# Kernel optimization log

Hardware: AMD Instinct MI355X
Metric: run time of the kernel (lower is better)

The kernel has to match this reference:

```python
import jax, jax.numpy as jnp
import numpy as np

D = 768          # hidden_size
N_HEADS = 12
HEAD_DIM = D // N_HEADS  # 64
WINDOW = 128 // 2        # local_attention // 2 = 64 tokens each side
ROPE_THETA = 10000.0     # local_rope_theta


def _rope_freqs(T, dtype=jnp.float32):
    # complex rotation factors e^{i * pos * inv_freq}, shape [T, HEAD_DIM//2]
    inv_freq = 1.0 / (ROPE_THETA ** (jnp.arange(0, HEAD_DIM, 2, dtype=dtype) / HEAD_DIM))
    ang = jnp.arange(T, dtype=dtype)[:, None] * inv_freq[None, :]
    return jnp.exp(1j * ang.astype(jnp.complex64))


def _apply_rope(x, freqs):
    # x: [B, T, N, H]; split into (2, H//2) pairs as in the source reshape
    B, T, N, H = x.shape
    pairs = x.reshape(B, T, N, 2, H // 2)
    c = pairs[..., 0, :] + 1j * pairs[..., 1, :]          # [B,T,N,H//2]
    rot = c * freqs[None, :, None, :]                      # broadcast over B, heads
    out = jnp.stack([jnp.real(rot), jnp.imag(rot)], axis=-1)  # [B,T,N,H//2,2]
    return out.reshape(B, T, N, H)  # attention_scaling = 1.0 for default rope


def setup_inputs() -> dict:
    key = jax.random.key(0)
    k1, k2, k3 = jax.random.split(key, 3)
    B, T = 4, 2048
    hidden_states = jax.random.normal(k1, (B, T, D), dtype=jnp.float32)
    attention_mask = jnp.ones((B, T), dtype=jnp.int32)
    Wqkv = jax.random.normal(k2, (3 * D, D), dtype=jnp.float32) * (1.0 / np.sqrt(D))
    Wo = jax.random.normal(k3, (D, D), dtype=jnp.float32) * (1.0 / np.sqrt(D))
    return {"hidden_states": hidden_states, "attention_mask": attention_mask,
            "Wqkv": Wqkv, "Wo": Wo}


def reference(hidden_states, attention_mask, Wqkv, Wo):
    B, T, _ = hidden_states.shape
    # fused QKV projection (no bias in ModernBERT)
    qkv = jnp.einsum('btd,ed->bte', hidden_states, Wqkv)   # [B,T,3D]
    q, k, v = jnp.split(qkv, 3, axis=-1)
    to_heads = lambda x: x.reshape(B, T, N_HEADS, HEAD_DIM)
    q, k, v = to_heads(q), to_heads(k), to_heads(v)
    # rotary embedding (complex multiply)
    freqs = _rope_freqs(T)
    q = _apply_rope(q, freqs)
    k = _apply_rope(k, freqs)
    # sliding-window + padding mask
    pos = jnp.arange(T)
    window = jnp.abs(pos[:, None] - pos[None, :]) <= WINDOW   # [T,T]
    pad = attention_mask.astype(jnp.bool_)                    # [B,T]
    allowed = window[None, None, :, :] & pad[:, None, :, None] & pad[:, None, None, :]
    # eager SDPA
    scale = 1.0 / np.sqrt(HEAD_DIM)
    scores = jnp.einsum('bqnh,bknh->bnqk', q, k) * scale      # [B,N,T,T]
    scores = jnp.where(allowed, scores, jnp.finfo(scores.dtype).min)
    probs = jax.nn.softmax(scores, axis=-1)
    attn = jnp.einsum('bnqk,bknh->bqnh', probs, v)            # [B,T,N,H]
    attn = attn.reshape(B, T, D)
    return jnp.einsum('btd,ed->bte', attn, Wo)                # output proj
```

## Files before the change

kernel.cpp:

```cpp
#include <hip/hip_runtime.h>
#include <hip/hip_bf16.h>
#include <math.h>

#define BATCH 4
#define SEQ   2048
#define DMODEL 768
#define NHEADS 12
#define HDIM  64
#define WIN   64
#define QKV_LD 2304

typedef __attribute__((ext_vector_type(8))) short bf16x8;
typedef __attribute__((ext_vector_type(4))) float f32x4;

typedef __attribute__((address_space(1))) const unsigned int guint;
typedef __attribute__((address_space(3))) unsigned int luint;

__device__ inline void gl_lds16(const __hip_bfloat16* g, __hip_bfloat16* l) {
    __builtin_amdgcn_global_load_lds((guint*)g, (luint*)l, 16, 0, 0);
}

__device__ inline void to_out(float* p, float v) { *p = v; }
__device__ inline void to_out(__hip_bfloat16* p, float v) { *p = __float2bfloat16(v); }

#define N4_HID  (BATCH * SEQ * DMODEL / 4)
#define N4_WQKV (QKV_LD * DMODEL / 4)
#define N4_WO   (DMODEL * DMODEL / 4)
#define N_ROPE  (SEQ * 32)
#define SETUP_TOTAL (N4_HID + N4_WQKV + N4_WO + N_ROPE)

__device__ inline void cast4(const float* in, __hip_bfloat16* out, int i) {
    float4 v = ((const float4*)in)[i];
    union { ushort4 u; __hip_bfloat16 h[4]; } o;
    o.h[0] = __float2bfloat16(v.x); o.h[1] = __float2bfloat16(v.y);
    o.h[2] = __float2bfloat16(v.z); o.h[3] = __float2bfloat16(v.w);
    ((ushort4*)out)[i] = o.u;
}

__global__ __launch_bounds__(256) void setup_kernel(const float* __restrict__ hidden,
                                                    const float* __restrict__ Wqkv,
                                                    const float* __restrict__ Wo,
                                                    __hip_bfloat16* __restrict__ hid_bf,
                                                    __hip_bfloat16* __restrict__ wqkv_bf,
                                                    __hip_bfloat16* __restrict__ wo_bf,
                                                    float2* __restrict__ tab) {
    int id = blockIdx.x * 256 + threadIdx.x;
    if (id < N4_HID) {
        cast4(hidden, hid_bf, id);
    } else if (id < N4_HID + N4_WQKV) {
        cast4(Wqkv, wqkv_bf, id - N4_HID);
    } else if (id < N4_HID + N4_WQKV + N4_WO) {
        cast4(Wo, wo_bf, id - N4_HID - N4_WQKV);
    } else if (id < SETUP_TOTAL) {
        int idx = id - (N4_HID + N4_WQKV + N4_WO);
        int t = idx >> 5, j = idx & 31;
        const float L2T_OVER_32 = 13.287712379549449f / 32.0f;
        float inv = exp2f(-(float)j * L2T_OVER_32);
        float s, c;
        sincosf((float)t * inv, &s, &c);
        tab[idx] = make_float2(c, s);
    }
}

template <typename OutT, bool ROPE>
__global__ __launch_bounds__(512) void gemm_pipe(const __hip_bfloat16* __restrict__ A,
                                                 const __hip_bfloat16* __restrict__ B,
                                                 OutT* __restrict__ C,
                                                 int lda, int ldb, int ldc,
                                                 const float2* __restrict__ rope_tab) {
    __shared__ __align__(16) char smem[131072];
    __hip_bfloat16* As = (__hip_bfloat16*)smem;
    __hip_bfloat16* Bs = (__hip_bfloat16*)(smem + 65536);

    const int tid  = threadIdx.x;
    const int lane = tid & 63;
    const int wave = tid >> 6;
    const int wm   = wave >> 1;
    const int wn   = wave & 1;
    const int fr   = lane & 15;
    const int quad = lane >> 4;

    const int bid = blockIdx.x;
    const int x   = bid & 7;
    const int j   = bid >> 3;
    const int m0  = (x * 8 + (j & 7)) * 128;
    const int n0  = (j >> 3) * 128;

    f32x4 acc[2][4];
#pragma unroll
    for (int i = 0; i < 2; i++)
#pragma unroll
        for (int jj = 0; jj < 4; jj++) acc[i][jj] = (f32x4){0.f, 0.f, 0.f, 0.f};

    auto stage = [&](int t) {
        const int s  = t & 3;
        const int k0 = t * 64;
#pragma unroll
        for (int c = 0; c < 2; ++c) {
            int tc  = c * 512 + tid;
            int row = tc >> 3, ch = tc & 7;
            int gcol = (ch ^ (row & 7)) * 8;
            gl_lds16(A + (size_t)(m0 + row) * lda + k0 + gcol, As + s * 8192 + tc * 8);
            gl_lds16(B + (size_t)(n0 + row) * ldb + k0 + gcol, Bs + s * 8192 + tc * 8);
        }
    };

    stage(0); stage(1); stage(2);

#pragma unroll
    for (int t = 0; t < 12; ++t) {
        if (t < 10)       asm volatile("s_waitcnt vmcnt(8)" ::: "memory");
        else if (t == 10) asm volatile("s_waitcnt vmcnt(4)" ::: "memory");
        else              asm volatile("s_waitcnt vmcnt(0)" ::: "memory");
        __builtin_amdgcn_s_barrier();
        __builtin_amdgcn_sched_barrier(0);

        if (t < 9) stage(t + 3);

        const __hip_bfloat16* as = As + (t & 3) * 8192;
        const __hip_bfloat16* bs = Bs + (t & 3) * 8192;
        bf16x8 af[2][2], bfv[2][4];
#pragma unroll
        for (int ks = 0; ks < 2; ++ks) {
#pragma unroll
            for (int mi = 0; mi < 2; ++mi) {
                int row = wm * 32 + mi * 16 + fr;
                int pos = (ks * 4 + quad) ^ (row & 7);
                af[ks][mi] = *(const bf16x8*)(as + row * 64 + pos * 8);
            }
#pragma unroll
            for (int ni = 0; ni < 4; ++ni) {
                int row = wn * 64 + ni * 16 + fr;
                int pos = (ks * 4 + quad) ^ (row & 7);
                bfv[ks][ni] = *(const bf16x8*)(bs + row * 64 + pos * 8);
            }
        }

        __builtin_amdgcn_s_setprio(1);
#pragma unroll
        for (int ks = 0; ks < 2; ++ks)
#pragma unroll
            for (int mi = 0; mi < 2; ++mi)
#pragma unroll
                for (int ni = 0; ni < 4; ++ni)
                    acc[mi][ni] = __builtin_amdgcn_mfma_f32_16x16x32_bf16(af[ks][mi], bfv[ks][ni], acc[mi][ni], 0, 0, 0);
        __builtin_amdgcn_s_setprio(0);
    }

    const int b0 = n0 + wn * 64;
    if (ROPE && b0 < 2 * DMODEL) {
#pragma unroll
        for (int mi = 0; mi < 2; mi++) {
#pragma unroll
            for (int r = 0; r < 4; r++) {
                int t = (m0 + wm * 32 + mi * 16 + quad * 4 + r) & (SEQ - 1);
#pragma unroll
                for (int ni = 0; ni < 2; ni++) {
                    float2 cs = rope_tab[t * 32 + ni * 16 + fr];
                    float x0 = acc[mi][ni][r], x1 = acc[mi][ni + 2][r];
                    acc[mi][ni][r]     = x0 * cs.x - x1 * cs.y;
                    acc[mi][ni + 2][r] = x0 * cs.y + x1 * cs.x;
                }
            }
        }
    }

#pragma unroll
    for (int mi = 0; mi < 2; mi++)
#pragma unroll
        for (int ni = 0; ni < 4; ni++) {
            f32x4 v = acc[mi][ni];
            int gc = b0 + ni * 16 + fr;
            size_t rbase = (size_t)(m0 + wm * 32 + mi * 16 + quad * 4);
#pragma unroll
            for (int r = 0; r < 4; r++)
                to_out(&C[(rbase + r) * ldc + gc], v[r]);
        }
}

#define PLD  192

__global__ __launch_bounds__(256) void attn_kernel(const __hip_bfloat16* __restrict__ qkv,
                                                   const int* __restrict__ mask,
                                                   __hip_bfloat16* __restrict__ attn) {
    __shared__ __align__(16) char smem[49152];
    __hip_bfloat16* Ks = (__hip_bfloat16*)smem;
    __hip_bfloat16* Pb = (__hip_bfloat16*)smem;
    __hip_bfloat16* Vt = (__hip_bfloat16*)(smem + 24576);

    const int tid  = threadIdx.x;
    const int lane = tid & 63;
    const int wave = tid >> 6;
    const int fr   = lane & 15;
    const int quad = lane >> 4;

    const int bid  = blockIdx.x;
    const int x    = bid & 7;
    const int j    = bid >> 3;
    const int b    = x >> 1;
    const int q0   = ((x & 1) * 16 + (j & 15)) * 64;
    const int head = j >> 4;

    const int klo = max(0, q0 - WIN);
    const int khi = min(SEQ, q0 + 64 + WIN);
    const int nk  = khi - klo;
    const int nt  = nk >> 4;
    const int nkc = nk >> 5;

    const size_t rowbase = (size_t)(b * SEQ) * QKV_LD + head * HDIM;

    for (int task = tid; task < nk * 8; task += 256) {
        int row = task >> 3, g = task & 7;
        uint4 v = *(const uint4*)(qkv + rowbase + (size_t)(klo + row) * QKV_LD + DMODEL + g * 8);
        *(uint4*)(Ks + row * 64 + (g ^ (row & 7)) * 8) = v;
    }
    {
        int h = lane;
        const __hip_bfloat16* vb = qkv + rowbase + 2 * DMODEL + h;
        int ng = nk >> 3;
        for (int g = wave; g < ng; g += 4) {
            unsigned int u0, u1, u2, u3;
            {
                unsigned short a0 = *(const unsigned short*)(vb + (size_t)(klo + g * 8 + 0) * QKV_LD);
                unsigned short a1 = *(const unsigned short*)(vb + (size_t)(klo + g * 8 + 1) * QKV_LD);
                unsigned short a2 = *(const unsigned short*)(vb + (size_t)(klo + g * 8 + 2) * QKV_LD);
                unsigned short a3 = *(const unsigned short*)(vb + (size_t)(klo + g * 8 + 3) * QKV_LD);
                unsigned short a4 = *(const unsigned short*)(vb + (size_t)(klo + g * 8 + 4) * QKV_LD);
                unsigned short a5 = *(const unsigned short*)(vb + (size_t)(klo + g * 8 + 5) * QKV_LD);
                unsigned short a6 = *(const unsigned short*)(vb + (size_t)(klo + g * 8 + 6) * QKV_LD);
                unsigned short a7 = *(const unsigned short*)(vb + (size_t)(klo + g * 8 + 7) * QKV_LD);
                u0 = (unsigned int)a0 | ((unsigned int)a1 << 16);
                u1 = (unsigned int)a2 | ((unsigned int)a3 << 16);
                u2 = (unsigned int)a4 | ((unsigned int)a5 << 16);
                u3 = (unsigned int)a6 | ((unsigned int)a7 << 16);
            }
            int cs = g ^ (h & 7);
            *(uint4*)(Vt + h * PLD + cs * 8) = make_uint4(u0, u1, u2, u3);
        }
    }

    const int qrow0 = q0 + wave * 16;
    bf16x8 aq0 = *(const bf16x8*)(qkv + rowbase + (size_t)(qrow0 + fr) * QKV_LD + quad * 8);
    bf16x8 aq1 = *(const bf16x8*)(qkv + rowbase + (size_t)(qrow0 + fr) * QKV_LD + 32 + quad * 8);

    const int* mb = mask + b * SEQ;
    int mq[4];
#pragma unroll
    for (int r = 0; r < 4; r++) mq[r] = mb[qrow0 + quad * 4 + r];

    __syncthreads();

    f32x4 sc[12];
#pragma unroll
    for (int kt = 0; kt < 12; kt++) sc[kt] = (f32x4){-1e30f, -1e30f, -1e30f, -1e30f};

#pragma unroll
    for (int kt = 0; kt < 12; kt++) {
        if (kt < nt) {
            int krow = kt * 16 + fr;
            int kg = klo + krow;
            int p0 = (quad) ^ (krow & 7);
            int p1 = (4 + quad) ^ (krow & 7);
            bf16x8 bk0 = *(const bf16x8*)(Ks + krow * 64 + p0 * 8);
            bf16x8 bk1 = *(const bf16x8*)(Ks + krow * 64 + p1 * 8);
            f32x4 a = (f32x4){0.f, 0.f, 0.f, 0.f};
            a = __builtin_amdgcn_mfma_f32_16x16x32_bf16(aq0, bk0, a, 0, 0, 0);
            a = __builtin_amdgcn_mfma_f32_16x16x32_bf16(aq1, bk1, a, 0, 0, 0);
            int mk = mb[kg];
            f32x4 s;
#pragma unroll
            for (int r = 0; r < 4; r++) {
                int qg = qrow0 + quad * 4 + r;
                bool ok = (abs(qg - kg) <= WIN) && (mk != 0) && (mq[r] != 0);
                s[r] = ok ? a[r] * 0.125f : -1e30f;
            }
            sc[kt] = s;
        }
    }

    f32x4 mx = sc[0];
#pragma unroll
    for (int kt = 1; kt < 12; kt++)
#pragma unroll
        for (int r = 0; r < 4; r++) mx[r] = fmaxf(mx[r], sc[kt][r]);
#pragma unroll
    for (int off = 8; off >= 1; off >>= 1)
#pragma unroll
        for (int r = 0; r < 4; r++) mx[r] = fmaxf(mx[r], __shfl_xor(mx[r], off));

    f32x4 sum = (f32x4){0.f, 0.f, 0.f, 0.f};
#pragma unroll
    for (int kt = 0; kt < 12; kt++)
#pragma unroll
        for (int r = 0; r < 4; r++) {
            float e = __expf(sc[kt][r] - mx[r]);
            sc[kt][r] = e;
            sum[r] += e;
        }
#pragma unroll
    for (int off = 8; off >= 1; off >>= 1)
#pragma unroll
        for (int r = 0; r < 4; r++) sum[r] += __shfl_xor(sum[r], off);
    f32x4 rs;
#pragma unroll
    for (int r = 0; r < 4; r++) rs[r] = 1.0f / sum[r];

    __syncthreads();
#pragma unroll
    for (int kt = 0; kt < 12; kt++) {
        if (kt < nt) {
#pragma unroll
            for (int r = 0; r < 4; r++) {
                int prow = wave * 16 + quad * 4 + r;
                int c = kt * 2 + (fr >> 3);
                int cs = c ^ (prow & 7);
                Pb[prow * PLD + cs * 8 + (fr & 7)] = __float2bfloat16(sc[kt][r] * rs[r]);
            }
        }
    }
    __syncthreads();

    f32x4 o[4];
#pragma unroll
    for (int ht = 0; ht < 4; ht++) o[ht] = (f32x4){0.f, 0.f, 0.f, 0.f};

#pragma unroll
    for (int kc = 0; kc < 6; kc++) {
        if (kc < nkc) {
            int cs = (kc * 4 + quad) ^ (fr & 7);
            bf16x8 ap = *(const bf16x8*)(Pb + (wave * 16 + fr) * PLD + cs * 8);
#pragma unroll
            for (int ht = 0; ht < 4; ht++) {
                bf16x8 bv = *(const bf16x8*)(Vt + (ht * 16 + fr) * PLD + cs * 8);
                o[ht] = __builtin_amdgcn_mfma_f32_16x16x32_bf16(ap, bv, o[ht], 0, 0, 0);
            }
        }
    }

    __hip_bfloat16* ob = attn + (size_t)(b * SEQ + qrow0) * DMODEL + head * HDIM;
#pragma unroll
    for (int r = 0; r < 4; r++)
#pragma unroll
        for (int ht = 0; ht < 4; ht++)
            ob[(size_t)(quad * 4 + r) * DMODEL + ht * 16 + fr] = __float2bfloat16(o[ht][r]);
}

extern "C" void kernel_launch(void* const* d_in, const int* in_sizes, int n_in,
                              void* d_out, int out_size, void* d_ws, size_t ws_size,
                              hipStream_t stream) {
    const float* hidden = (const float*)d_in[0];
    const int*   mask   = (const int*)d_in[1];
    const float* Wqkv   = (const float*)d_in[2];
    const float* Wo     = (const float*)d_in[3];
    float* out = (float*)d_out;

    char* w = (char*)d_ws;
    __hip_bfloat16* qkv_bf  = (__hip_bfloat16*)(w);
    __hip_bfloat16* hid_bf  = (__hip_bfloat16*)(w + 37748736);
    __hip_bfloat16* wqkv_bf = (__hip_bfloat16*)(w + 50331648);
    __hip_bfloat16* wo_bf   = (__hip_bfloat16*)(w + 53870592);
    __hip_bfloat16* attn_bf = (__hip_bfloat16*)(w + 55050240);
    float2*         tab     = (float2*)(w + 67633152);

    setup_kernel<<<SETUP_TOTAL / 256, 256, 0, stream>>>(hidden, Wqkv, Wo,
                                                        hid_bf, wqkv_bf, wo_bf, tab);

    gemm_pipe<__hip_bfloat16, true><<<18 * 64, 512, 0, stream>>>(hid_bf, wqkv_bf, qkv_bf,
                                                                 DMODEL, DMODEL, QKV_LD, tab);

    attn_kernel<<<(SEQ / 64) * NHEADS * BATCH, 256, 0, stream>>>(qkv_bf, mask, attn_bf);

    gemm_pipe<float, false><<<6 * 64, 512, 0, stream>>>(attn_bf, wo_bf, out,
                                                        DMODEL, DMODEL, DMODEL, nullptr);
}
```

Measured before the change: 170.3 us.

## Replace 4-stage 512-thread GEMM pipeline with 256-thread double-buffered GEMM

Reworks the projection GEMM from a 512-thread, 4-stage LDS ring into a 256-thread double-buffered kernel. Each wave now computes a 64x64 sub-tile instead of 32x64. LDS use drops from 128KB to 64KB, so more blocks may fit per CU. The trade-off is shallower prefetch, an extra barrier per k-step, and more accumulator registers per thread, which could expose global-load latency or lower occupancy.

```diff
diff --git a/kernel.cpp b/kernel.cpp
--- a/kernel.cpp
+++ b/kernel.cpp
@@ -63,14 +63,14 @@
 }
 
 template <typename OutT, bool ROPE>
-__global__ __launch_bounds__(512) void gemm_pipe(const __hip_bfloat16* __restrict__ A,
-                                                 const __hip_bfloat16* __restrict__ B,
-                                                 OutT* __restrict__ C,
-                                                 int lda, int ldb, int ldc,
-                                                 const float2* __restrict__ rope_tab) {
-    __shared__ __align__(16) char smem[131072];
+__global__ __launch_bounds__(256) void gemm_db(const __hip_bfloat16* __restrict__ A,
+                                               const __hip_bfloat16* __restrict__ B,
+                                               OutT* __restrict__ C,
+                                               int lda, int ldb, int ldc,
+                                               const float2* __restrict__ rope_tab) {
+    __shared__ __align__(16) char smem[65536];
     __hip_bfloat16* As = (__hip_bfloat16*)smem;
-    __hip_bfloat16* Bs = (__hip_bfloat16*)(smem + 65536);
+    __hip_bfloat16* Bs = (__hip_bfloat16*)(smem + 32768);
 
     const int tid  = threadIdx.x;
     const int lane = tid & 63;
@@ -86,74 +86,80 @@
     const int m0  = (x * 8 + (j & 7)) * 128;
     const int n0  = (j >> 3) * 128;
 
-    f32x4 acc[2][4];
-#pragma unroll
-    for (int i = 0; i < 2; i++)
+    f32x4 acc[4][4];
+#pragma unroll
+    for (int i = 0; i < 4; i++)
 #pragma unroll
         for (int jj = 0; jj < 4; jj++) acc[i][jj] = (f32x4){0.f, 0.f, 0.f, 0.f};
 
     auto stage = [&](int t) {
-        const int s  = t & 3;
+        const int s  = t & 1;
         const int k0 = t * 64;
 #pragma unroll
-        for (int c = 0; c < 2; ++c) {
-            int tc  = c * 512 + tid;
+        for (int c = 0; c < 4; ++c) {
+            int tc  = (wave * 4 + c) * 64 + lane;
             int row = tc >> 3, ch = tc & 7;
             int gcol = (ch ^ (row & 7)) * 8;
             gl_lds16(A + (size_t)(m0 + row) * lda + k0 + gcol, As + s * 8192 + tc * 8);
+        }
+#pragma unroll
+        for (int c = 0; c < 4; ++c) {
+            int tc  = (wave * 4 + c) * 64 + lane;
+            int row = tc >> 3, ch = tc & 7;
+            int gcol = (ch ^ (row & 7)) * 8;
             gl_lds16(B + (size_t)(n0 + row) * ldb + k0 + gcol, Bs + s * 8192 + tc * 8);
         }
     };
 
-    stage(0); stage(1); stage(2);
+    stage(0); stage(1);
 
 #pragma unroll
     for (int t = 0; t < 12; ++t) {
-        if (t < 10)       asm volatile("s_waitcnt vmcnt(8)" ::: "memory");
-        else if (t == 10) asm volatile("s_waitcnt vmcnt(4)" ::: "memory");
-        else              asm volatile("s_waitcnt vmcnt(0)" ::: "memory");
+        if (t < 11) asm volatile("s_waitcnt vmcnt(8)" ::: "memory");
+        else        asm volatile("s_waitcnt vmcnt(0)" ::: "memory");
         __builtin_amdgcn_s_barrier();
         __builtin_amdgcn_sched_barrier(0);
 
-        if (t < 9) stage(t + 3);
-
-        const __hip_bfloat16* as = As + (t & 3) * 8192;
-        const __hip_bfloat16* bs = Bs + (t & 3) * 8192;
-        bf16x8 af[2][2], bfv[2][4];
+        const __hip_bfloat16* as = As + (t & 1) * 8192;
+        const __hip_bfloat16* bs = Bs + (t & 1) * 8192;
 #pragma unroll
         for (int ks = 0; ks < 2; ++ks) {
-#pragma unroll
-            for (int mi = 0; mi < 2; ++mi) {
-                int row = wm * 32 + mi * 16 + fr;
+            bf16x8 af[4], bfv[4];
+#pragma unroll
+            for (int mi = 0; mi < 4; ++mi) {
+                int row = wm * 64 + mi * 16 + fr;
                 int pos = (ks * 4 + quad) ^ (row & 7);
-                af[ks][mi] = *(const bf16x8*)(as + row * 64 + pos * 8);
+                af[mi] = *(const bf16x8*)(as + row * 64 + pos * 8);
             }
 #pragma unroll
             for (int ni = 0; ni < 4; ++ni) {
                 int row = wn * 64 + ni * 16 + fr;
                 int pos = (ks * 4 + quad) ^ (row & 7);
-                bfv[ks][ni] = *(const bf16x8*)(bs + row * 64 + pos * 8);
-            }
-        }
-
-        __builtin_amdgcn_s_setprio(1);
-#pragma unroll
-        for (int ks = 0; ks < 2; ++ks)
-#pragma unroll
-            for (int mi = 0; mi < 2; ++mi)
+                bfv[ni] = *(const bf16x8*)(bs + row * 64 + pos * 8);
+            }
+            __builtin_amdgcn_s_setprio(1);
+#pragma unroll
+            for (int mi = 0; mi < 4; ++mi)
 #pragma unroll
                 for (int ni = 0; ni < 4; ++ni)
-                    acc[mi][ni] = __builtin_amdgcn_mfma_f32_16x16x32_bf16(af[ks][mi], bfv[ks][ni], acc[mi][ni], 0, 0, 0);
-        __builtin_amdgcn_s_setprio(0);
+                    acc[mi][ni] = __builtin_amdgcn_mfma_f32_16x16x32_bf16(af[mi], bfv[ni], acc[mi][ni], 0, 0, 0);
+            __builtin_amdgcn_s_setprio(0);
+        }
+
+        if (t < 10) {
+            __builtin_amdgcn_s_barrier();
+            __builtin_amdgcn_sched_barrier(0);
+            stage(t + 2);
+        }
     }
 
     const int b0 = n0 + wn * 64;
     if (ROPE && b0 < 2 * DMODEL) {
 #pragma unroll
-        for (int mi = 0; mi < 2; mi++) {
+        for (int mi = 0; mi < 4; mi++) {
 #pragma unroll
             for (int r = 0; r < 4; r++) {
-                int t = (m0 + wm * 32 + mi * 16 + quad * 4 + r) & (SEQ - 1);
+                int t = (m0 + wm * 64 + mi * 16 + quad * 4 + r) & (SEQ - 1);
 #pragma unroll
                 for (int ni = 0; ni < 2; ni++) {
                     float2 cs = rope_tab[t * 32 + ni * 16 + fr];
@@ -166,12 +172,12 @@
     }
 
 #pragma unroll
-    for (int mi = 0; mi < 2; mi++)
+    for (int mi = 0; mi < 4; mi++)
 #pragma unroll
         for (int ni = 0; ni < 4; ni++) {
             f32x4 v = acc[mi][ni];
             int gc = b0 + ni * 16 + fr;
-            size_t rbase = (size_t)(m0 + wm * 32 + mi * 16 + quad * 4);
+            size_t rbase = (size_t)(m0 + wm * 64 + mi * 16 + quad * 4);
 #pragma unroll
             for (int r = 0; r < 4; r++)
                 to_out(&C[(rbase + r) * ldc + gc], v[r]);
@@ -365,11 +371,11 @@
     setup_kernel<<<SETUP_TOTAL / 256, 256, 0, stream>>>(hidden, Wqkv, Wo,
                                                         hid_bf, wqkv_bf, wo_bf, tab);
 
-    gemm_pipe<__hip_bfloat16, true><<<18 * 64, 512, 0, stream>>>(hid_bf, wqkv_bf, qkv_bf,
-                                                                 DMODEL, DMODEL, QKV_LD, tab);
+    gemm_db<__hip_bfloat16, true><<<18 * 64, 256, 0, stream>>>(hid_bf, wqkv_bf, qkv_bf,
+                                                               DMODEL, DMODEL, QKV_LD, tab);
 
     attn_kernel<<<(SEQ / 64) * NHEADS * BATCH, 256, 0, stream>>>(qkv_bf, mask, attn_bf);
 
-    gemm_pipe<float, false><<<6 * 64, 512, 0, stream>>>(attn_bf, wo_bf, out,
-                                                        DMODEL, DMODEL, DMODEL, nullptr);
-}
+    gemm_db<float, false><<<6 * 64, 256, 0, stream>>>(attn_bf, wo_bf, out,
+                                                      DMODEL, DMODEL, DMODEL, nullptr);
+}
```

Measured after the change: 167.7 us. No clear change (-1.6%).
